# Optimization experiments

Measured on AMD Instinct MI355X. Metric: run time of the kernel, lower is better.

Reference implementation:

```python
import jax, jax.numpy as jnp
import numpy as np

UNITS = 512
INPUT_DIM = 64
BATCH = 131072


def setup_inputs() -> dict:
    key = jax.random.key(0)
    kx, kw = jax.random.split(key)
    x = jax.random.normal(kx, (BATCH, INPUT_DIM), dtype=jnp.float32)
    w = jax.random.normal(kw, (UNITS, INPUT_DIM), dtype=jnp.float32) * 0.05
    return {"x": x, "w": w}


def reference(x, w):
    # Pairwise squared L2 distance: dist[b, u] = sum_d (w[u,d] - x[b,d])^2
    # avoids the O(B*U*D) broadcast intermediate).
    x_sq = jnp.sum(x * x, axis=-1, keepdims=True)        # [B, 1]
    w_sq = jnp.sum(w * w, axis=-1)[None, :]              # [1, U]
    cross = jnp.einsum("bd,ud->bu", x, w)                # [B, U]
    return x_sq + w_sq - 2.0 * cross
```

## Files before the change

kernel.cpp:

```cpp
#include <hip/hip_runtime.h>

#define BATCH 131072
#define UNITS 512
#define DIM   64
#define BM    128
#define STRIDE 68

typedef __attribute__((ext_vector_type(8))) short  short8;
typedef __attribute__((ext_vector_type(4))) float  floatx4;

static __device__ __forceinline__ unsigned short f32_to_bf16(float f) {
    union { float f; unsigned int u; } c; c.f = f;
    unsigned int u = c.u;
    unsigned int r = u + 0x7fffu + ((u >> 16) & 1u);
    return (unsigned short)(r >> 16);
}

__global__ __launch_bounds__(256) void prep_w_kernel(
    const float* __restrict__ w,
    unsigned short* __restrict__ wb,
    float* __restrict__ wsq)
{
    const int u = blockIdx.x * 4 + (threadIdx.x >> 6);
    const int d = threadIdx.x & 63;
    float v = w[u * DIM + d];
    wb[u * DIM + d] = f32_to_bf16(v);
    float s = v * v;
    #pragma unroll
    for (int o = 32; o > 0; o >>= 1) s += __shfl_xor(s, o);
    if (d == 0) wsq[u] = s;
}

__global__ __launch_bounds__(256) void dist_kernel(
    const float* __restrict__ x,
    const unsigned short* __restrict__ wb,
    const float* __restrict__ wsq,
    float* __restrict__ out)
{
    __shared__ __align__(16) unsigned short xb[BM][DIM];
    __shared__ float xsq[BM];
    __shared__ float wsq_s[UNITS];
    __shared__ __align__(16) float st[4][16][STRIDE];

    const int tid  = threadIdx.x;
    const int row0 = blockIdx.x * BM;

    wsq_s[tid]       = wsq[tid];
    wsq_s[tid + 256] = wsq[tid + 256];

    #pragma unroll
    for (int half = 0; half < BM / 64; ++half) {
        const int r = half * 64 + (tid >> 2);
        const int q = tid & 3;
        const float4* src = (const float4*)(x + (size_t)(row0 + r) * DIM + q * 16);
        float v[16];
        *(float4*)&v[0]  = src[0];
        *(float4*)&v[4]  = src[1];
        *(float4*)&v[8]  = src[2];
        *(float4*)&v[12] = src[3];
        float s = 0.f;
        unsigned short p[16];
        #pragma unroll
        for (int i = 0; i < 16; ++i) { s += v[i] * v[i]; p[i] = f32_to_bf16(v[i]); }
        uint4* dst = (uint4*)&xb[r][q * 16];
        dst[0] = *(uint4*)&p[0];
        dst[1] = *(uint4*)&p[8];
        s += __shfl_xor(s, 1);
        s += __shfl_xor(s, 2);
        if (q == 0) xsq[r] = s;
    }
    __syncthreads();

    const int wave = tid >> 6;
    const int lane = tid & 63;
    const int l15  = lane & 15;
    const int quad = lane >> 4;
    const int mrow = wave * 32;

    short8 a[2][2];
    float  xs[2][4];
    #pragma unroll
    for (int mf = 0; mf < 2; ++mf) {
        const short8* ar = (const short8*)&xb[mrow + mf * 16 + l15][0];
        a[mf][0] = ar[quad];
        a[mf][1] = ar[quad + 4];
        #pragma unroll
        for (int i = 0; i < 4; ++i)
            xs[mf][i] = xsq[mrow + mf * 16 + quad * 4 + i];
    }

    const short8* wv  = (const short8*)wb;
    float*        stw = &st[wave][0][0];

    for (int gu = 0; gu < 8; ++gu) {
        const int colb = gu * 64;

        short8 b[4][2];
        float  wq[4];
        #pragma unroll
        for (int t = 0; t < 4; ++t) {
            const short8* bp = wv + (size_t)(colb + t * 16 + l15) * 8;
            b[t][0] = bp[quad];
            b[t][1] = bp[quad + 4];
            wq[t]   = wsq_s[colb + t * 16 + l15];
        }

        #pragma unroll
        for (int mf = 0; mf < 2; ++mf) {
            floatx4 acc[4];
            #pragma unroll
            for (int t = 0; t < 4; ++t) {
                acc[t] = floatx4{0.f, 0.f, 0.f, 0.f};
                acc[t] = __builtin_amdgcn_mfma_f32_16x16x32_bf16(a[mf][0], b[t][0], acc[t], 0, 0, 0);
                acc[t] = __builtin_amdgcn_mfma_f32_16x16x32_bf16(a[mf][1], b[t][1], acc[t], 0, 0, 0);
            }

            #pragma unroll
            for (int t = 0; t < 4; ++t)
                #pragma unroll
                for (int i = 0; i < 4; ++i)
                    stw[(quad * 4 + i) * STRIDE + t * 16 + l15] =
                        xs[mf][i] + wq[t] - 2.0f * acc[t][i];

            #pragma unroll
            for (int j = 0; j < 4; ++j) {
                const int r = quad + 4 * j;
                const floatx4 v = *(const floatx4*)&stw[r * STRIDE + l15 * 4];
                float* dst = out + (size_t)(row0 + mrow + mf * 16 + r) * UNITS
                                 + colb + l15 * 4;
                __builtin_nontemporal_store(v, (floatx4*)dst);
            }
        }
    }
}

extern "C" void kernel_launch(void* const* d_in, const int* in_sizes, int n_in,
                              void* d_out, int out_size, void* d_ws, size_t ws_size,
                              hipStream_t stream) {
    const float* x = (const float*)d_in[0];
    const float* w = (const float*)d_in[1];
    float* out = (float*)d_out;

    unsigned short* wb  = (unsigned short*)d_ws;
    float*          wsq = (float*)((char*)d_ws + UNITS * DIM * 2);

    prep_w_kernel<<<UNITS / 4, 256, 0, stream>>>(w, wb, wsq);
    dist_kernel<<<BATCH / BM, 256, 0, stream>>>(x, wb, wsq, out);
}
```

Baseline: 293.9 us.

## Swap MFMA operands to store output directly and load x straight to registers

Swaps the A/B operands of the MFMA so each lane's accumulator holds four consecutive output columns of one row. The result can then be written straight to global memory as a float4, with no LDS staging transpose. It also drops the LDS staging of x: each lane loads its bf16 fragment directly from global memory and computes the row norm with cross-quad shuffles. This removes LDS traffic and the staging buffer, which may raise occupancy. The cost is less contiguous global stores, since each row only gets 64-byte segments per instruction, and the direct x loads are less coalesced.

```diff
diff --git a/kernel.cpp b/kernel.cpp
--- a/kernel.cpp
+++ b/kernel.cpp
@@ -4,7 +4,6 @@
 #define UNITS 512
 #define DIM   64
 #define BM    128
-#define STRIDE 68
 
 typedef __attribute__((ext_vector_type(8))) short  short8;
 typedef __attribute__((ext_vector_type(4))) float  floatx4;
@@ -37,38 +36,13 @@
     const float* __restrict__ wsq,
     float* __restrict__ out)
 {
-    __shared__ __align__(16) unsigned short xb[BM][DIM];
-    __shared__ float xsq[BM];
-    __shared__ float wsq_s[UNITS];
-    __shared__ __align__(16) float st[4][16][STRIDE];
+    __shared__ __align__(16) float wsq_s[UNITS];
 
     const int tid  = threadIdx.x;
     const int row0 = blockIdx.x * BM;
 
     wsq_s[tid]       = wsq[tid];
     wsq_s[tid + 256] = wsq[tid + 256];
-
-    #pragma unroll
-    for (int half = 0; half < BM / 64; ++half) {
-        const int r = half * 64 + (tid >> 2);
-        const int q = tid & 3;
-        const float4* src = (const float4*)(x + (size_t)(row0 + r) * DIM + q * 16);
-        float v[16];
-        *(float4*)&v[0]  = src[0];
-        *(float4*)&v[4]  = src[1];
-        *(float4*)&v[8]  = src[2];
-        *(float4*)&v[12] = src[3];
-        float s = 0.f;
-        unsigned short p[16];
-        #pragma unroll
-        for (int i = 0; i < 16; ++i) { s += v[i] * v[i]; p[i] = f32_to_bf16(v[i]); }
-        uint4* dst = (uint4*)&xb[r][q * 16];
-        dst[0] = *(uint4*)&p[0];
-        dst[1] = *(uint4*)&p[8];
-        s += __shfl_xor(s, 1);
-        s += __shfl_xor(s, 2);
-        if (q == 0) xsq[r] = s;
-    }
     __syncthreads();
 
     const int wave = tid >> 6;
@@ -78,57 +52,57 @@
     const int mrow = wave * 32;
 
     short8 a[2][2];
-    float  xs[2][4];
+    float  xs2[2];
     #pragma unroll
     for (int mf = 0; mf < 2; ++mf) {
-        const short8* ar = (const short8*)&xb[mrow + mf * 16 + l15][0];
-        a[mf][0] = ar[quad];
-        a[mf][1] = ar[quad + 4];
+        const float* xr = x + (size_t)(row0 + mrow + mf * 16 + l15) * DIM;
+        float v[16];
+        *(float4*)&v[0]  = *(const float4*)(xr + quad * 8);
+        *(float4*)&v[4]  = *(const float4*)(xr + quad * 8 + 4);
+        *(float4*)&v[8]  = *(const float4*)(xr + 32 + quad * 8);
+        *(float4*)&v[12] = *(const float4*)(xr + 32 + quad * 8 + 4);
+        float s = 0.f;
+        unsigned short p[16];
         #pragma unroll
-        for (int i = 0; i < 4; ++i)
-            xs[mf][i] = xsq[mrow + mf * 16 + quad * 4 + i];
+        for (int i = 0; i < 16; ++i) { s += v[i] * v[i]; p[i] = f32_to_bf16(v[i]); }
+        a[mf][0] = *(short8*)&p[0];
+        a[mf][1] = *(short8*)&p[8];
+        s += __shfl_xor(s, 16);
+        s += __shfl_xor(s, 32);
+        xs2[mf] = s;
     }
 
-    const short8* wv  = (const short8*)wb;
-    float*        stw = &st[wave][0][0];
+    const short8* wv = (const short8*)wb;
 
     for (int gu = 0; gu < 8; ++gu) {
         const int colb = gu * 64;
 
-        short8 b[4][2];
-        float  wq[4];
+        short8  b[4][2];
+        floatx4 wq[4];
         #pragma unroll
         for (int t = 0; t < 4; ++t) {
             const short8* bp = wv + (size_t)(colb + t * 16 + l15) * 8;
             b[t][0] = bp[quad];
             b[t][1] = bp[quad + 4];
-            wq[t]   = wsq_s[colb + t * 16 + l15];
+            wq[t]   = *(const floatx4*)&wsq_s[colb + t * 16 + quad * 4];
         }
 
         #pragma unroll
         for (int mf = 0; mf < 2; ++mf) {
-            floatx4 acc[4];
             #pragma unroll
             for (int t = 0; t < 4; ++t) {
-                acc[t] = floatx4{0.f, 0.f, 0.f, 0.f};
-                acc[t] = __builtin_amdgcn_mfma_f32_16x16x32_bf16(a[mf][0], b[t][0], acc[t], 0, 0, 0);
-                acc[t] = __builtin_amdgcn_mfma_f32_16x16x32_bf16(a[mf][1], b[t][1], acc[t], 0, 0, 0);
-            }
+                floatx4 acc = floatx4{0.f, 0.f, 0.f, 0.f};
+                acc = __builtin_amdgcn_mfma_f32_16x16x32_bf16(b[t][0], a[mf][0], acc, 0, 0, 0);
+                acc = __builtin_amdgcn_mfma_f32_16x16x32_bf16(b[t][1], a[mf][1], acc, 0, 0, 0);
 
-            #pragma unroll
-            for (int t = 0; t < 4; ++t)
+                floatx4 vo;
                 #pragma unroll
                 for (int i = 0; i < 4; ++i)
-                    stw[(quad * 4 + i) * STRIDE + t * 16 + l15] =
-                        xs[mf][i] + wq[t] - 2.0f * acc[t][i];
+                    vo[i] = xs2[mf] + wq[t][i] - 2.0f * acc[i];
 
-            #pragma unroll
-            for (int j = 0; j < 4; ++j) {
-                const int r = quad + 4 * j;
-                const floatx4 v = *(const floatx4*)&stw[r * STRIDE + l15 * 4];
-                float* dst = out + (size_t)(row0 + mrow + mf * 16 + r) * UNITS
-                                 + colb + l15 * 4;
-                __builtin_nontemporal_store(v, (floatx4*)dst);
+                float* dst = out + (size_t)(row0 + mrow + mf * 16 + l15) * UNITS
+                                 + colb + t * 16 + quad * 4;
+                __builtin_nontemporal_store(vo, (floatx4*)dst);
             }
         }
     }
```

Measured after the change: 328.4 us. 11.7% more time.
